# Kernel tuning notes

Hardware: AMD Instinct MI355X
Metric: run time of the kernel (lower is better)

The kernel has to match this reference:

```python
import jax, jax.numpy as jnp
import numpy as np

E, P, T, B = 512, 128, 1024, 1


def _lstm_dir(x, wih, whh, bih, bhh, reverse):
    # x: [B, T, Din]; torch LSTM gate order: i, f, g, o
    Bb = x.shape[0]
    H = whh.shape[1]
    xg = jnp.einsum('btd,gd->btg', x, wih) + bih + bhh  # [B, T, 4H]
    xg = jnp.swapaxes(xg, 0, 1)  # [T, B, 4H]

    def step(carry, g_t):
        h, c = carry
        g = g_t + h @ whh.T
        i, f, gg, o = jnp.split(g, 4, axis=-1)
        c = jax.nn.sigmoid(f) * c + jax.nn.sigmoid(i) * jnp.tanh(gg)
        h = jax.nn.sigmoid(o) * jnp.tanh(c)
        return (h, c), h

    h0 = jnp.zeros((Bb, H), x.dtype)
    _, hs = jax.lax.scan(step, (h0, h0), xg, reverse=reverse)
    return jnp.swapaxes(hs, 0, 1)  # [B, T, H]


def _bilstm(x, layers):
    for wih, whh, bih, bhh in layers:
        f = _lstm_dir(x, wih[0], whh[0], bih[0], bhh[0], False)
        b = _lstm_dir(x, wih[1], whh[1], bih[1], bhh[1], True)
        x = jnp.concatenate([f, b], axis=-1)
    return x


def setup_inputs() -> dict:
    key = jax.random.key(0)
    ks = jax.random.split(key, 20)
    s = 0.05
    d = {
        'words': jax.random.normal(ks[0], (B, T, E), jnp.float32),
        'pos': jax.random.normal(ks[1], (B, T, P), jnp.float32),
        'w_w0_ih': s * jax.random.normal(ks[2], (2, 4 * E, E), jnp.float32),
        'w_w0_hh': s * jax.random.normal(ks[3], (2, 4 * E, E), jnp.float32),
        'w_b0_ih': s * jax.random.normal(ks[4], (2, 4 * E), jnp.float32),
        'w_b0_hh': s * jax.random.normal(ks[5], (2, 4 * E), jnp.float32),
        'w_w1_ih': s * jax.random.normal(ks[6], (2, 4 * E, 2 * E), jnp.float32),
        'w_w1_hh': s * jax.random.normal(ks[7], (2, 4 * E, E), jnp.float32),
        'w_b1_ih': s * jax.random.normal(ks[8], (2, 4 * E), jnp.float32),
        'w_b1_hh': s * jax.random.normal(ks[9], (2, 4 * E), jnp.float32),
        'p_w0_ih': s * jax.random.normal(ks[10], (2, 4 * P, P), jnp.float32),
        'p_w0_hh': s * jax.random.normal(ks[11], (2, 4 * P, P), jnp.float32),
        'p_b0_ih': s * jax.random.normal(ks[12], (2, 4 * P), jnp.float32),
        'p_b0_hh': s * jax.random.normal(ks[13], (2, 4 * P), jnp.float32),
        'p_w1_ih': s * jax.random.normal(ks[14], (2, 4 * P, 2 * P), jnp.float32),
        'p_w1_hh': s * jax.random.normal(ks[15], (2, 4 * P, P), jnp.float32),
        'p_b1_ih': s * jax.random.normal(ks[16], (2, 4 * P), jnp.float32),
        'p_b1_hh': s * jax.random.normal(ks[17], (2, 4 * P), jnp.float32),
        'edge_w': s * jax.random.normal(ks[18], (1, 4 * (E + P)), jnp.float32),
        'edge_b': s * jax.random.normal(ks[19], (1,), jnp.float32),
    }
    return d


def reference(words, pos, w_w0_ih, w_w0_hh, w_b0_ih, w_b0_hh, w_w1_ih, w_w1_hh,
              w_b1_ih, w_b1_hh, p_w0_ih, p_w0_hh, p_b0_ih, p_b0_hh, p_w1_ih,
              p_w1_hh, p_b1_ih, p_b1_hh, edge_w, edge_b):
    hw = _bilstm(words, [(w_w0_ih, w_w0_hh, w_b0_ih, w_b0_hh),
                         (w_w1_ih, w_w1_hh, w_b1_ih, w_b1_hh)])  # [B,T,2E]
    hp = _bilstm(pos, [(p_w0_ih, p_w0_hh, p_b0_ih, p_b0_hh),
                       (p_w1_ih, p_w1_hh, p_b1_ih, p_b1_hh)])    # [B,T,2P]
    H = jnp.concatenate([hw, hp], axis=-1)[0]  # [T, 2(E+P)]
    D = H.shape[-1]
    # edge_scorer(concat(h_i, h_j)) = h_i @ W1 + h_j @ W2 + b
    s1 = H @ edge_w[0, :D]  # [T]
    s2 = H @ edge_w[0, D:]  # [T]
    S = s1[:, None] + s2[None, :] + edge_b[0]
    n = H.shape[0]
    eye = jnp.eye(n, dtype=bool)
    return jnp.where(eye, jnp.zeros((), S.dtype), S)  # diagonal stays 0
```

## Files before the change

kernel.cpp:

```cpp
#include <hip/hip_runtime.h>


#define T_LEN 1024

__global__ void poison_kernel(unsigned* p, int n) {
  int i = blockIdx.x * blockDim.x + threadIdx.x;
  int stride = gridDim.x * blockDim.x;
  for (; i < n; i += stride) p[i] = 0xFFFFFFFFu;
}

__global__ __launch_bounds__(256) void gemm_bt(
    const float* __restrict__ A,
    const float* __restrict__ Wt,
    const float* __restrict__ B0,
    const float* __restrict__ B1,
    float* __restrict__ C,
    int M, int N, int K)
{
  const int z = blockIdx.z;
  const float* W  = Wt + (size_t)z * N * K;
  const float* b0 = B0 + (size_t)z * N;
  const float* b1 = B1 + (size_t)z * N;
  float* Cz = C + (size_t)z * M * N;

  __shared__ __align__(16) float As[16][64];
  __shared__ __align__(16) float Ws[16][64];

  const int tid = threadIdx.x;
  const int tx = tid & 15, ty = tid >> 4;
  const int brow = blockIdx.y * 64, bcol = blockIdx.x * 64;
  const int lr = tid >> 2;
  const int lk = (tid & 3) << 2;

  float acc[4][4] = {};

  for (int k0 = 0; k0 < K; k0 += 16) {
    float4 av = *(const float4*)(A + (size_t)(brow + lr) * K + k0 + lk);
    float4 wv = *(const float4*)(W + (size_t)(bcol + lr) * K + k0 + lk);
    __syncthreads();
    As[lk + 0][lr] = av.x; As[lk + 1][lr] = av.y;
    As[lk + 2][lr] = av.z; As[lk + 3][lr] = av.w;
    Ws[lk + 0][lr] = wv.x; Ws[lk + 1][lr] = wv.y;
    Ws[lk + 2][lr] = wv.z; Ws[lk + 3][lr] = wv.w;
    __syncthreads();
    #pragma unroll
    for (int kk = 0; kk < 16; ++kk) {
      float4 a = *(const float4*)&As[kk][ty << 2];
      float4 w = *(const float4*)&Ws[kk][tx << 2];
      float a4[4] = {a.x, a.y, a.z, a.w};
      float w4[4] = {w.x, w.y, w.z, w.w};
      #pragma unroll
      for (int i = 0; i < 4; ++i)
        #pragma unroll
        for (int j = 0; j < 4; ++j)
          acc[i][j] = fmaf(a4[i], w4[j], acc[i][j]);
    }
  }

  const int nb = bcol + (tx << 2);
  float bias[4];
  #pragma unroll
  for (int j = 0; j < 4; ++j) bias[j] = b0[nb + j] + b1[nb + j];
  #pragma unroll
  for (int i = 0; i < 4; ++i) {
    int m = brow + (ty << 2) + i;
    float4 out;
    out.x = acc[i][0] + bias[0];
    out.y = acc[i][1] + bias[1];
    out.z = acc[i][2] + bias[2];
    out.w = acc[i][3] + bias[3];
    *(float4*)(Cz + (size_t)m * N + nb) = out;
  }
}

__device__ __forceinline__ float fsigmoid(float x) {
  return 1.f / (1.f + __expf(-x));
}
__device__ __forceinline__ float ftanh(float x) {
  return 2.f / (1.f + __expf(-2.f * x)) - 1.f;
}

template<int CTRL>
__device__ __forceinline__ float dpp_add(float v) {
  int x = __builtin_amdgcn_update_dpp(0, __float_as_int(v), CTRL, 0xf, 0xf, true);
  return v + __int_as_float(x);
}

__device__ __forceinline__ void word_body(
    int wg, const float* __restrict__ xg, const float* __restrict__ whh,
    float* hbuf, int rev)
{
  const int tid  = threadIdx.x;
  const int wave = tid >> 6;
  const int lane = tid & 63;
  const int p    = lane & 31;
  const int half = lane >> 5;
  const int eloc = wave * 2 + half;
  const int e    = wg * 16 + eloc;

  float4 wv[4][4];
  #pragma unroll
  for (int g = 0; g < 4; ++g) {
    const float* row = whh + (size_t)(g * 512 + e) * 512 + 4 * p;
    #pragma unroll
    for (int k = 0; k < 4; ++k)
      wv[g][k] = *(const float4*)(row + 128 * k);
  }

  __shared__ __align__(16) float h_lds[512];
  __shared__ __align__(16) float4 hgates[16];

  unsigned* hb = (unsigned*)hbuf;

  const bool tail = (tid < 16);
  float cst = 0.f;
  float xg4[4] = {0.f, 0.f, 0.f, 0.f};
  if (tail) {
    const int t0 = rev ? (T_LEN - 1) : 0;
    #pragma unroll
    for (int g = 0; g < 4; ++g)
      xg4[g] = xg[(size_t)t0 * 2048 + g * 512 + wg * 16 + tid];
  }

  unsigned A = 0, B = 0, C = 0;

  for (int s = 0; s < T_LEN; ++s) {
    const int t = rev ? (T_LEN - 1 - s) : s;

    if (s == 0) {
      h_lds[tid] = 0.f;
    } else {
      const int tp = rev ? (t + 1) : (t - 1);
      const unsigned* addr = hb + (size_t)tp * 512 + tid;
      asm volatile(
          "s_waitcnt vmcnt(0)\n\t"
          "global_load_dword %0, %3, off sc0 sc1\n\t"
          "global_load_dword %1, %3, off sc0 sc1\n\t"
          "global_load_dword %2, %3, off sc0 sc1\n\t"
          "Lpoll%=:\n\t"
          "s_waitcnt vmcnt(2)\n\t"
          "v_cmp_eq_u32 vcc, -1, %0\n\t"
          "s_cbranch_vccz Ldone%=\n\t"
          "global_load_dword %0, %3, off sc0 sc1\n\t"
          "s_waitcnt vmcnt(2)\n\t"
          "v_cmp_eq_u32 vcc, -1, %1\n\t"
          "s_cbranch_vccz LuseB%=\n\t"
          "global_load_dword %1, %3, off sc0 sc1\n\t"
          "s_waitcnt vmcnt(2)\n\t"
          "v_cmp_eq_u32 vcc, -1, %2\n\t"
          "s_cbranch_vccz LuseC%=\n\t"
          "global_load_dword %2, %3, off sc0 sc1\n\t"
          "s_branch Lpoll%=\n\t"
          "LuseB%=:\n\t"
          "v_mov_b32 %0, %1\n\t"
          "s_branch Ldone%=\n\t"
          "LuseC%=:\n\t"
          "v_mov_b32 %0, %2\n\t"
          "Ldone%=:"
          : "+v"(A), "+v"(B), "+v"(C)
          : "v"(addr)
          : "vcc", "memory");
      h_lds[tid] = __uint_as_float(A);
    }
    __syncthreads();

    float a0 = 0.f, a1 = 0.f, a2 = 0.f, a3 = 0.f;
    #pragma unroll
    for (int k = 0; k < 4; ++k) {
      float4 hv = *(const float4*)&h_lds[128 * k + 4 * p];
      float h4[4] = {hv.x, hv.y, hv.z, hv.w};
      #pragma unroll
      for (int j = 0; j < 4; ++j) {
        a0 = fmaf(((const float*)&wv[0][k])[j], h4[j], a0);
        a1 = fmaf(((const float*)&wv[1][k])[j], h4[j], a1);
        a2 = fmaf(((const float*)&wv[2][k])[j], h4[j], a2);
        a3 = fmaf(((const float*)&wv[3][k])[j], h4[j], a3);
      }
    }

    a0 = dpp_add<0xB1>(a0);  a1 = dpp_add<0xB1>(a1);
    a2 = dpp_add<0xB1>(a2);  a3 = dpp_add<0xB1>(a3);
    a0 = dpp_add<0x4E>(a0);  a1 = dpp_add<0x4E>(a1);
    a2 = dpp_add<0x4E>(a2);  a3 = dpp_add<0x4E>(a3);
    a0 = dpp_add<0x141>(a0); a1 = dpp_add<0x141>(a1);
    a2 = dpp_add<0x141>(a2); a3 = dpp_add<0x141>(a3);
    a0 = dpp_add<0x140>(a0); a1 = dpp_add<0x140>(a1);
    a2 = dpp_add<0x140>(a2); a3 = dpp_add<0x140>(a3);
    a0 = dpp_add<0x142>(a0); a1 = dpp_add<0x142>(a1);
    a2 = dpp_add<0x142>(a2); a3 = dpp_add<0x142>(a3);

    if (p == 16) {
      float4 gsum; gsum.x = a0; gsum.y = a1; gsum.z = a2; gsum.w = a3;
      hgates[eloc] = gsum;
    }
    __syncthreads();

    if (tail) {
      float4 g4 = hgates[tid];
      float si = fsigmoid(g4.x + xg4[0]);
      float sf = fsigmoid(g4.y + xg4[1]);
      float tg = ftanh  (g4.z + xg4[2]);
      float so = fsigmoid(g4.w + xg4[3]);
      cst = fmaf(sf, cst, si * tg);
      float h = so * ftanh(cst);
      __hip_atomic_store(hb + (size_t)t * 512 + wg * 16 + tid,
                         __float_as_uint(h),
                         __ATOMIC_RELAXED, __HIP_MEMORY_SCOPE_AGENT);
      if (s + 1 < T_LEN) {
        const int tn = rev ? (t - 1) : (t + 1);
        #pragma unroll
        for (int g = 0; g < 4; ++g)
          xg4[g] = xg[(size_t)tn * 2048 + g * 512 + wg * 16 + tid];
      }
    }
  }

  asm volatile("s_waitcnt vmcnt(0)" : "+v"(A), "+v"(B), "+v"(C) :: "memory");
}

__device__ __forceinline__ void pos_body(
    const float* __restrict__ xg, const float* __restrict__ whh,
    float* __restrict__ hbuf, int rev)
{
  const int tid = threadIdx.x;
  const int p   = tid & 3;
  const int e   = tid >> 2;

  float w[4][32];
  #pragma unroll
  for (int g = 0; g < 4; ++g) {
    const float* row = whh + (size_t)(g * 128 + e) * 128 + 4 * p;
    #pragma unroll
    for (int k = 0; k < 8; ++k) {
      float4 v = *(const float4*)(row + 16 * k);
      w[g][k * 4 + 0] = v.x; w[g][k * 4 + 1] = v.y;
      w[g][k * 4 + 2] = v.z; w[g][k * 4 + 3] = v.w;
    }
  }

  __shared__ __align__(16) float h_lds[2][128];

  float cst = 0.f;
  float xg4[4] = {0.f, 0.f, 0.f, 0.f};
  if (p == 0) {
    const int t0 = rev ? (T_LEN - 1) : 0;
    #pragma unroll
    for (int g = 0; g < 4; ++g) xg4[g] = xg[(size_t)t0 * 512 + g * 128 + e];
  }
  if (tid < 128) h_lds[0][tid] = 0.f;
  __syncthreads();

  for (int s = 0; s < T_LEN; ++s) {
    const int t   = rev ? (T_LEN - 1 - s) : s;
    const int buf = s & 1;

    float a0 = 0.f, a1 = 0.f, a2 = 0.f, a3 = 0.f;
    #pragma unroll
    for (int k = 0; k < 8; ++k) {
      float4 hv = *(const float4*)&h_lds[buf][16 * k + 4 * p];
      float h4[4] = {hv.x, hv.y, hv.z, hv.w};
      #pragma unroll
      for (int j = 0; j < 4; ++j) {
        a0 = fmaf(w[0][k * 4 + j], h4[j], a0);
        a1 = fmaf(w[1][k * 4 + j], h4[j], a1);
        a2 = fmaf(w[2][k * 4 + j], h4[j], a2);
        a3 = fmaf(w[3][k * 4 + j], h4[j], a3);
      }
    }
    a0 = dpp_add<0xB1>(a0); a1 = dpp_add<0xB1>(a1);
    a2 = dpp_add<0xB1>(a2); a3 = dpp_add<0xB1>(a3);
    a0 = dpp_add<0x4E>(a0); a1 = dpp_add<0x4E>(a1);
    a2 = dpp_add<0x4E>(a2); a3 = dpp_add<0x4E>(a3);

    if (p == 0) {
      float si = fsigmoid(a0 + xg4[0]);
      float sf = fsigmoid(a1 + xg4[1]);
      float tg = ftanh  (a2 + xg4[2]);
      float so = fsigmoid(a3 + xg4[3]);
      cst = fmaf(sf, cst, si * tg);
      float h = so * ftanh(cst);
      h_lds[buf ^ 1][e] = h;
      hbuf[(size_t)t * 128 + e] = h;
      if (s + 1 < T_LEN) {
        const int tn = rev ? (t - 1) : (t + 1);
        #pragma unroll
        for (int g = 0; g < 4; ++g)
          xg4[g] = xg[(size_t)tn * 512 + g * 128 + e];
      }
    }
    __syncthreads();
  }
}

__global__ __launch_bounds__(512, 1) void rec_kernel(
    const float* xg_wf, const float* xg_wb, const float* whh_w,
    float* h_wf, float* h_wb,
    const float* xg_pf, const float* xg_pb, const float* whh_p,
    float* h_pf, float* h_pb)
{
  int b = blockIdx.x;
  if (b < 32)
    word_body(b, xg_wf, whh_w, h_wf, 0);
  else if (b < 64)
    word_body(b - 32, xg_wb, whh_w + 2048 * 512, h_wb, 1);
  else if (b == 64)
    pos_body(xg_pf, whh_p, h_pf, 0);
  else
    pos_body(xg_pb, whh_p + 512 * 128, h_pb, 1);
}

__global__ void concat_k(const float* __restrict__ wf, const float* __restrict__ wb,
                         const float* __restrict__ pf, const float* __restrict__ pb,
                         float* __restrict__ wcat, float* __restrict__ pcat)
{
  const int totw = T_LEN * 1024;
  const int totp = T_LEN * 256;
  int idx = blockIdx.x * blockDim.x + threadIdx.x;
  int stride = gridDim.x * blockDim.x;
  for (int e = idx; e < totw + totp; e += stride) {
    if (e < totw) {
      int t = e >> 10, d = e & 1023;
      wcat[e] = d < 512 ? wf[t * 512 + d] : wb[t * 512 + (d - 512)];
    } else {
      int e2 = e - totw;
      int t = e2 >> 8, d = e2 & 255;
      pcat[e2] = d < 128 ? pf[t * 128 + d] : pb[t * 128 + (d - 128)];
    }
  }
}

__global__ __launch_bounds__(256) void edge_s(
    const float* __restrict__ hwf, const float* __restrict__ hwb,
    const float* __restrict__ hpf, const float* __restrict__ hpb,
    const float* __restrict__ ew, float* s1, float* s2)
{
  const int i = blockIdx.x;
  const int tid = threadIdx.x;
  float a1 = 0.f, a2 = 0.f;
  for (int d = tid; d < 1280; d += 256) {
    float hv;
    if (d < 512)       hv = hwf[i * 512 + d];
    else if (d < 1024) hv = hwb[i * 512 + d - 512];
    else if (d < 1152) hv = hpf[i * 128 + d - 1024];
    else               hv = hpb[i * 128 + d - 1152];
    a1 = fmaf(hv, ew[d], a1);
    a2 = fmaf(hv, ew[1280 + d], a2);
  }
  #pragma unroll
  for (int off = 32; off > 0; off >>= 1) {
    a1 += __shfl_xor(a1, off, 64);
    a2 += __shfl_xor(a2, off, 64);
  }
  __shared__ float r1[4], r2[4];
  const int wid = tid >> 6;
  if ((tid & 63) == 0) { r1[wid] = a1; r2[wid] = a2; }
  __syncthreads();
  if (tid == 0) {
    s1[i] = (r1[0] + r1[1]) + (r1[2] + r1[3]);
    s2[i] = (r2[0] + r2[1]) + (r2[2] + r2[3]);
  }
}

__global__ __launch_bounds__(256) void sfill(
    const float* __restrict__ s1, const float* __restrict__ s2,
    const float* __restrict__ eb, float* __restrict__ out)
{
  int e = blockIdx.x * 256 + threadIdx.x;
  int i = e >> 10, j = e & 1023;
  out[e] = (i == j) ? 0.f : s1[i] + s2[j] + eb[0];
}

extern "C" void kernel_launch(void* const* d_in, const int* in_sizes, int n_in,
                              void* d_out, int out_size, void* d_ws, size_t ws_size,
                              hipStream_t stream)
{
  const float* words   = (const float*)d_in[0];
  const float* pos     = (const float*)d_in[1];
  const float* w_w0_ih = (const float*)d_in[2];
  const float* w_w0_hh = (const float*)d_in[3];
  const float* w_b0_ih = (const float*)d_in[4];
  const float* w_b0_hh = (const float*)d_in[5];
  const float* w_w1_ih = (const float*)d_in[6];
  const float* w_w1_hh = (const float*)d_in[7];
  const float* w_b1_ih = (const float*)d_in[8];
  const float* w_b1_hh = (const float*)d_in[9];
  const float* p_w0_ih = (const float*)d_in[10];
  const float* p_w0_hh = (const float*)d_in[11];
  const float* p_b0_ih = (const float*)d_in[12];
  const float* p_b0_hh = (const float*)d_in[13];
  const float* p_w1_ih = (const float*)d_in[14];
  const float* p_w1_hh = (const float*)d_in[15];
  const float* p_b1_ih = (const float*)d_in[16];
  const float* p_b1_hh = (const float*)d_in[17];
  const float* edge_w  = (const float*)d_in[18];
  const float* edge_b  = (const float*)d_in[19];

  float* ws = (float*)d_ws;
  float* xg_w  = ws;
  float* xg_p  = ws + 4194304;
  float* hw0_f = ws + 5242880;
  float* hw0_b = hw0_f + 524288;
  float* hw1_f = hw0_b + 524288;
  float* hw1_b = hw1_f + 524288;
  float* hp0_f = hw1_b + 524288;
  float* hp0_b = hp0_f + 131072;
  float* hp1_f = hp0_b + 131072;
  float* hp1_b = hp1_f + 131072;
  float* wcat  = hp1_b + 131072;
  float* pcat  = wcat + 1048576;
  float* s1    = pcat + 262144;
  float* s2    = s1 + 1024;

  poison_kernel<<<1024, 256, 0, stream>>>((unsigned*)hw0_f, 2097152);

  gemm_bt<<<dim3(32, 16, 2), 256, 0, stream>>>(words, w_w0_ih, w_b0_ih, w_b0_hh,
                                               xg_w, 1024, 2048, 512);
  gemm_bt<<<dim3(8, 16, 2), 256, 0, stream>>>(pos, p_w0_ih, p_b0_ih, p_b0_hh,
                                              xg_p, 1024, 512, 128);

  rec_kernel<<<66, 512, 0, stream>>>(xg_w, xg_w + 2097152, w_w0_hh, hw0_f, hw0_b,
                                     xg_p, xg_p + 524288, p_w0_hh, hp0_f, hp0_b);

  concat_k<<<2048, 256, 0, stream>>>(hw0_f, hw0_b, hp0_f, hp0_b, wcat, pcat);

  gemm_bt<<<dim3(32, 16, 2), 256, 0, stream>>>(wcat, w_w1_ih, w_b1_ih, w_b1_hh,
                                               xg_w, 1024, 2048, 1024);
  gemm_bt<<<dim3(8, 16, 2), 256, 0, stream>>>(pcat, p_w1_ih, p_b1_ih, p_b1_hh,
                                              xg_p, 1024, 512, 256);

  rec_kernel<<<66, 512, 0, stream>>>(xg_w, xg_w + 2097152, w_w1_hh, hw1_f, hw1_b,
                                     xg_p, xg_p + 524288, p_w1_hh, hp1_f, hp1_b);

  edge_s<<<1024, 256, 0, stream>>>(hw1_f, hw1_b, hp1_f, hp1_b, edge_w, s1, s2);
  sfill<<<4096, 256, 0, stream>>>(s1, s2, edge_b, (float*)d_out);
}
```

Baseline: 3.357 ms.

## Overlap layer-1 input GEMM with layer-0 recurrence via poisoned-row dataflow

The layer-0 recurrent kernel gains extra blocks that compute the layer-1 input projection tile by tile. Each tile spin-waits on poisoned sentinel values until both the forward and backward hidden rows it needs have been written, then writes its result into the same xg buffers that layer 0 has already consumed. This removes the separate concat kernel and the two layer-1 GEMM launches, and hides that GEMM under the serial recurrence. In exchange, hidden-state writes become agent-scope atomic stores, correctness depends on the poison fill and the row ordering, and the extra blocks may compete with the recurrent blocks for memory bandwidth.

```diff
diff --git a/kernel.cpp b/kernel.cpp
--- a/kernel.cpp
+++ b/kernel.cpp
@@ -239,6 +239,7 @@
   }
 
   __shared__ __align__(16) float h_lds[2][128];
+  unsigned* hb = (unsigned*)hbuf;
 
   float cst = 0.f;
   float xg4[4] = {0.f, 0.f, 0.f, 0.f};
@@ -280,7 +281,8 @@
       cst = fmaf(sf, cst, si * tg);
       float h = so * ftanh(cst);
       h_lds[buf ^ 1][e] = h;
-      hbuf[(size_t)t * 128 + e] = h;
+      __hip_atomic_store(hb + (size_t)t * 128 + e, __float_as_uint(h),
+                         __ATOMIC_RELAXED, __HIP_MEMORY_SCOPE_AGENT);
       if (s + 1 < T_LEN) {
         const int tn = rev ? (t - 1) : (t + 1);
         #pragma unroll
@@ -292,39 +294,134 @@
   }
 }
 
+__device__ const int rtorder[16] = {7,8,6,9,5,10,4,11,3,12,2,13,1,14,0,15};
+
+__device__ __forceinline__ void wait_rows(const unsigned* rowF,
+                                          const unsigned* rowB, int width) {
+  const int tid = threadIdx.x;
+  if (tid < width) {
+    while (__hip_atomic_load(rowF + tid, __ATOMIC_RELAXED,
+                             __HIP_MEMORY_SCOPE_AGENT) == 0xFFFFFFFFu)
+      __builtin_amdgcn_s_sleep(8);
+    while (__hip_atomic_load(rowB + tid, __ATOMIC_RELAXED,
+                             __HIP_MEMORY_SCOPE_AGENT) == 0xFFFFFFFFu)
+      __builtin_amdgcn_s_sleep(8);
+  }
+  __syncthreads();
+}
+
+__device__ __forceinline__ void df_tile(
+    const float* __restrict__ Alo, const float* __restrict__ Ahi, int ksplit,
+    int K, const float* __restrict__ W,
+    const float* __restrict__ b0, const float* __restrict__ b1,
+    float* __restrict__ C, int N, int brow, int bcol)
+{
+  __shared__ __align__(16) float As[16][64];
+  __shared__ __align__(16) float Ws[16][64];
+
+  const int tid = threadIdx.x;
+  const int tx = tid & 15, ty = (tid >> 4) & 15;
+  const int lr = (tid >> 2) & 63;
+  const int lk = (tid & 3) << 2;
+
+  float acc[4][4] = {};
+
+  for (int k0 = 0; k0 < K; k0 += 16) {
+    float4 av, wv;
+    if (tid < 256) {
+      const int k = k0 + lk;
+      const float* arow = (k < ksplit)
+          ? (Alo + (size_t)(brow + lr) * ksplit + k)
+          : (Ahi + (size_t)(brow + lr) * ksplit + (k - ksplit));
+      av = *(const float4*)arow;
+      wv = *(const float4*)(W + (size_t)(bcol + lr) * K + k0 + lk);
+    }
+    __syncthreads();
+    if (tid < 256) {
+      As[lk + 0][lr] = av.x; As[lk + 1][lr] = av.y;
+      As[lk + 2][lr] = av.z; As[lk + 3][lr] = av.w;
+      Ws[lk + 0][lr] = wv.x; Ws[lk + 1][lr] = wv.y;
+      Ws[lk + 2][lr] = wv.z; Ws[lk + 3][lr] = wv.w;
+    }
+    __syncthreads();
+    if (tid < 256) {
+      #pragma unroll
+      for (int kk = 0; kk < 16; ++kk) {
+        float4 a = *(const float4*)&As[kk][ty << 2];
+        float4 w = *(const float4*)&Ws[kk][tx << 2];
+        float a4[4] = {a.x, a.y, a.z, a.w};
+        float w4[4] = {w.x, w.y, w.z, w.w};
+        #pragma unroll
+        for (int i = 0; i < 4; ++i)
+          #pragma unroll
+          for (int j = 0; j < 4; ++j)
+            acc[i][j] = fmaf(a4[i], w4[j], acc[i][j]);
+      }
+    }
+  }
+
+  if (tid < 256) {
+    const int nb = bcol + (tx << 2);
+    float bias[4];
+    #pragma unroll
+    for (int j = 0; j < 4; ++j) bias[j] = b0[nb + j] + b1[nb + j];
+    #pragma unroll
+    for (int i = 0; i < 4; ++i) {
+      int m = brow + (ty << 2) + i;
+      float4 out;
+      out.x = acc[i][0] + bias[0];
+      out.y = acc[i][1] + bias[1];
+      out.z = acc[i][2] + bias[2];
+      out.w = acc[i][3] + bias[3];
+      *(float4*)(C + (size_t)m * N + nb) = out;
+    }
+  }
+}
+
 __global__ __launch_bounds__(512, 1) void rec_kernel(
     const float* xg_wf, const float* xg_wb, const float* whh_w,
     float* h_wf, float* h_wb,
     const float* xg_pf, const float* xg_pb, const float* whh_p,
-    float* h_pf, float* h_pb)
-{
-  int b = blockIdx.x;
-  if (b < 32)
+    float* h_pf, float* h_pb,
+    const float* w1_ih, const float* w1_b0, const float* w1_b1, float* xg1_w,
+    const float* p1_ih, const float* p1_b0, const float* p1_b1, float* xg1_p)
+{
+  const int b = blockIdx.x;
+  if (b < 32) {
     word_body(b, xg_wf, whh_w, h_wf, 0);
-  else if (b < 64)
+  } else if (b < 64) {
     word_body(b - 32, xg_wb, whh_w + 2048 * 512, h_wb, 1);
-  else if (b == 64)
+  } else if (b == 64) {
     pos_body(xg_pf, whh_p, h_pf, 0);
-  else
+  } else if (b == 65) {
     pos_body(xg_pb, whh_p + 512 * 128, h_pb, 1);
-}
-
-__global__ void concat_k(const float* __restrict__ wf, const float* __restrict__ wb,
-                         const float* __restrict__ pf, const float* __restrict__ pb,
-                         float* __restrict__ wcat, float* __restrict__ pcat)
-{
-  const int totw = T_LEN * 1024;
-  const int totp = T_LEN * 256;
-  int idx = blockIdx.x * blockDim.x + threadIdx.x;
-  int stride = gridDim.x * blockDim.x;
-  for (int e = idx; e < totw + totp; e += stride) {
-    if (e < totw) {
-      int t = e >> 10, d = e & 1023;
-      wcat[e] = d < 512 ? wf[t * 512 + d] : wb[t * 512 + (d - 512)];
-    } else {
-      int e2 = e - totw;
-      int t = e2 >> 8, d = e2 & 255;
-      pcat[e2] = d < 128 ? pf[t * 128 + d] : pb[t * 128 + (d - 128)];
+  } else if (b < 194) {
+    const int g = b - 66;
+    for (int j = g; j < 1024; j += 128) {
+      const int rti = rtorder[j >> 6];
+      const int rem = j & 63;
+      const int z = rem >> 5, ct = rem & 31;
+      const int brow = rti * 64, bcol = ct * 64;
+      wait_rows((const unsigned*)(h_wf + (size_t)(brow + 63) * 512),
+                (const unsigned*)(h_wb + (size_t)brow * 512), 512);
+      df_tile(h_wf, h_wb, 512, 1024,
+              w1_ih + (size_t)z * 2048 * 1024,
+              w1_b0 + z * 2048, w1_b1 + z * 2048,
+              xg1_w + (size_t)z * 1024 * 2048, 2048, brow, bcol);
+    }
+  } else {
+    const int g = b - 194;
+    for (int j = g; j < 256; j += 8) {
+      const int rti = rtorder[j >> 4];
+      const int rem = j & 15;
+      const int z = rem >> 3, ct = rem & 7;
+      const int brow = rti * 64, bcol = ct * 64;
+      wait_rows((const unsigned*)(h_pf + (size_t)(brow + 63) * 128),
+                (const unsigned*)(h_pb + (size_t)brow * 128), 128);
+      df_tile(h_pf, h_pb, 128, 256,
+              p1_ih + (size_t)z * 512 * 256,
+              p1_b0 + z * 512, p1_b1 + z * 512,
+              xg1_p + (size_t)z * 1024 * 512, 512, brow, bcol);
     }
   }
 }
@@ -406,30 +503,27 @@
   float* hp0_b = hp0_f + 131072;
   float* hp1_f = hp0_b + 131072;
   float* hp1_b = hp1_f + 131072;
-  float* wcat  = hp1_b + 131072;
-  float* pcat  = wcat + 1048576;
-  float* s1    = pcat + 262144;
+  float* s1    = hp1_b + 131072;
   float* s2    = s1 + 1024;
 
-  poison_kernel<<<1024, 256, 0, stream>>>((unsigned*)hw0_f, 2097152);
+  poison_kernel<<<1024, 256, 0, stream>>>((unsigned*)hw0_f, 2359296);
 
   gemm_bt<<<dim3(32, 16, 2), 256, 0, stream>>>(words, w_w0_ih, w_b0_ih, w_b0_hh,
                                                xg_w, 1024, 2048, 512);
   gemm_bt<<<dim3(8, 16, 2), 256, 0, stream>>>(pos, p_w0_ih, p_b0_ih, p_b0_hh,
                                               xg_p, 1024, 512, 128);
 
-  rec_kernel<<<66, 512, 0, stream>>>(xg_w, xg_w + 2097152, w_w0_hh, hw0_f, hw0_b,
-                                     xg_p, xg_p + 524288, p_w0_hh, hp0_f, hp0_b);
-
-  concat_k<<<2048, 256, 0, stream>>>(hw0_f, hw0_b, hp0_f, hp0_b, wcat, pcat);
-
-  gemm_bt<<<dim3(32, 16, 2), 256, 0, stream>>>(wcat, w_w1_ih, w_b1_ih, w_b1_hh,
-                                               xg_w, 1024, 2048, 1024);
-  gemm_bt<<<dim3(8, 16, 2), 256, 0, stream>>>(pcat, p_w1_ih, p_b1_ih, p_b1_hh,
-                                              xg_p, 1024, 512, 256);
-
-  rec_kernel<<<66, 512, 0, stream>>>(xg_w, xg_w + 2097152, w_w1_hh, hw1_f, hw1_b,
-                                     xg_p, xg_p + 524288, p_w1_hh, hp1_f, hp1_b);
+  rec_kernel<<<202, 512, 0, stream>>>(
+      xg_w, xg_w + 2097152, w_w0_hh, hw0_f, hw0_b,
+      xg_p, xg_p + 524288, p_w0_hh, hp0_f, hp0_b,
+      w_w1_ih, w_b1_ih, w_b1_hh, xg_w,
+      p_w1_ih, p_b1_ih, p_b1_hh, xg_p);
+
+  rec_kernel<<<66, 512, 0, stream>>>(
+      xg_w, xg_w + 2097152, w_w1_hh, hw1_f, hw1_b,
+      xg_p, xg_p + 524288, p_w1_hh, hp1_f, hp1_b,
+      w_w1_ih, w_b1_ih, w_b1_hh, xg_w,
+      p_w1_ih, p_b1_ih, p_b1_hh, xg_p);
 
   edge_s<<<1024, 256, 0, stream>>>(hw1_f, hw1_b, hp1_f, hp1_b, edge_w, s1, s2);
   sfill<<<4096, 256, 0, stream>>>(s1, s2, edge_b, (float*)d_out);
```

Result: faster. 3.249 ms (-3.2%).
